# Kernel optimization log

Hardware: AMD Instinct MI355X
Metric: run time of the kernel (lower is better)

Reference implementation:

```python
import jax, jax.numpy as jnp
import numpy as np

D_MODEL = 2048
NUM_HEADS = 32
NUM_KV_HEADS = 8
D_K = D_MODEL // NUM_HEADS
B, S = 2, 2048


def setup_inputs() -> dict:
    key = jax.random.key(0)
    ks = jax.random.split(key, 6)
    sc = 1.0 / np.sqrt(D_MODEL)
    x = jax.random.normal(ks[0], (B, S, D_MODEL), dtype=jnp.float32)
    mask = jnp.tril(jnp.ones((S, S), dtype=jnp.float32))[None, None]  # [1,1,S,S]
    return {
        'x': x,
        'mask': mask,
        'Wq': jax.random.normal(ks[1], (D_MODEL, D_MODEL), jnp.float32) * sc,
        'bq': jnp.zeros((D_MODEL,), jnp.float32),
        'Wk': jax.random.normal(ks[2], (D_MODEL, NUM_KV_HEADS * D_K), jnp.float32) * sc,
        'bk': jnp.zeros((NUM_KV_HEADS * D_K,), jnp.float32),
        'Wv': jax.random.normal(ks[3], (D_MODEL, NUM_KV_HEADS * D_K), jnp.float32) * sc,
        'bv': jnp.zeros((NUM_KV_HEADS * D_K,), jnp.float32),
        'Wo': jax.random.normal(ks[4], (D_MODEL, D_MODEL), jnp.float32) * sc,
        'bo': jnp.zeros((D_MODEL,), jnp.float32),
    }


def reference(x, mask, Wq, bq, Wk, bk, Wv, bv, Wo, bo):
    b, s, _ = x.shape
    g = NUM_HEADS // NUM_KV_HEADS  # queries per kv head
    Q = (x @ Wq + bq).reshape(b, s, NUM_HEADS, D_K).transpose(0, 2, 1, 3)      # [b,h,s,dk]
    K = (x @ Wk + bk).reshape(b, s, NUM_KV_HEADS, D_K).transpose(0, 2, 1, 3)   # [b,kv,s,dk]
    V = (x @ Wv + bv).reshape(b, s, NUM_KV_HEADS, D_K).transpose(0, 2, 1, 3)
    # group queries per kv head instead of repeat_interleave on K/V
    Qg = Q.reshape(b, NUM_KV_HEADS, g, s, D_K)
    scores = jnp.einsum('bkgqd,bkld->bkgql', Qg, K) / np.sqrt(D_K)             # [b,kv,g,s,s]
    scores = jnp.where(mask[:, :, None] == 0, -1e9, scores)
    attn = jax.nn.softmax(scores, axis=-1)
    out = jnp.einsum('bkgql,bkld->bkgqd', attn, V)                              # [b,kv,g,s,dk]
    out = out.reshape(b, NUM_HEADS, s, D_K).transpose(0, 2, 1, 3).reshape(b, s, D_MODEL)
    return out @ Wo + bo
```

## Files before the change

### kernel.cpp

```cpp
#include <hip/hip_runtime.h>
#include <stdint.h>

typedef __bf16 bf16x8 __attribute__((ext_vector_type(8)));
typedef float  f32x4  __attribute__((ext_vector_type(4)));

__device__ __forceinline__ f32x4 mfma16(bf16x8 a, bf16x8 b, f32x4 c) {
    return __builtin_amdgcn_mfma_f32_16x16x32_bf16(a, b, c, 0, 0, 0);
}

__device__ __forceinline__ uint16_t f2bf(float f) {
    union { __bf16 b; uint16_t u; } cv; cv.b = (__bf16)f; return cv.u;
}

typedef __attribute__((address_space(3))) void as3_void;
typedef __attribute__((address_space(1))) void as1_void;
__device__ __forceinline__ void async_ld16(const void* g, void* l) {
    __builtin_amdgcn_global_load_lds((const as1_void*)g, (as3_void*)l, 16, 0, 0);
}


__global__ void convert_f32_bf16(const float* __restrict__ in, uint16_t* __restrict__ out, int n) {
    int i = (blockIdx.x * 256 + threadIdx.x) * 4;
    if (i >= n) return;
    float4 v = *(const float4*)(in + i);
    ushort4 o;
    o.x = f2bf(v.x); o.y = f2bf(v.y); o.z = f2bf(v.z); o.w = f2bf(v.w);
    *(ushort4*)(out + i) = o;
}

__global__ void transpose_f32_bf16(const float* __restrict__ in, uint16_t* __restrict__ out,
                                   int ldin, int out_off, int ldout) {
    __shared__ float tile[32][33];
    const int c0 = blockIdx.x << 5, r0 = blockIdx.y << 5;
    const int tx = threadIdx.x, ty = threadIdx.y;
#pragma unroll
    for (int i = 0; i < 4; ++i)
        tile[ty + i * 8][tx] = in[(size_t)(r0 + ty + i * 8) * ldin + c0 + tx];
    __syncthreads();
#pragma unroll
    for (int i = 0; i < 4; ++i)
        out[(size_t)(out_off + c0 + ty + i * 8) * ldout + r0 + tx] = f2bf(tile[tx][ty + i * 8]);
}

__global__ void transpose_v(const uint16_t* __restrict__ qkv, uint16_t* __restrict__ vt) {
    __shared__ uint16_t tile[32][33];
    const int c0 = blockIdx.x << 5, r0 = blockIdx.y << 5, b = blockIdx.z;
    const int tx = threadIdx.x, ty = threadIdx.y;
#pragma unroll
    for (int i = 0; i < 4; ++i)
        tile[ty + i * 8][tx] = qkv[(size_t)(b * 2048 + r0 + ty + i * 8) * 3072 + 2560 + c0 + tx];
    __syncthreads();
    const int perm = 4 * (tx >> 3) + (((tx & 7) < 4) ? 0 : 16) + (tx & 3);
#pragma unroll
    for (int i = 0; i < 4; ++i)
        vt[(size_t)(b * 512 + c0 + ty + i * 8) * 2048 + r0 + tx] = tile[perm][ty + i * 8];
}

__global__ void concat_bias(const float* __restrict__ bq, const float* __restrict__ bk,
                            const float* __restrict__ bv, float* __restrict__ out) {
    int i = blockIdx.x * 256 + threadIdx.x;
    if (i >= 3072) return;
    out[i] = (i < 2048) ? bq[i] : (i < 2560 ? bk[i - 2048] : bv[i - 2560]);
}

template <bool F32OUT>
__global__ __launch_bounds__(256, 2)
void gemm_bt(const uint16_t* __restrict__ A, const uint16_t* __restrict__ Bt,
             const float* __restrict__ bias, void* __restrict__ Cout, int N, int K) {
    __shared__ __align__(16) uint16_t As[4096];
    __shared__ __align__(16) uint16_t Bs[4096];
    const int tid = threadIdx.x;
    const int wv = tid >> 6, ln = tid & 63;
    const int quad = ln >> 4, l16 = ln & 15;
    const int row0 = blockIdx.y << 7, col0 = blockIdx.x << 7;
    const int wm = wv >> 1, wn = wv & 1;

    const int p0 = tid, p1 = tid + 256;
    const int ar0 = p0 >> 2, ac0 = (p0 & 3) ^ ((ar0 ^ (ar0 >> 2)) & 3);
    const int ar1 = p1 >> 2, ac1 = (p1 & 3) ^ ((ar1 ^ (ar1 >> 2)) & 3);
    const uint16_t* gA0 = A + (size_t)(row0 + ar0) * K + (ac0 << 3);
    const uint16_t* gA1 = A + (size_t)(row0 + ar1) * K + (ac1 << 3);
    const uint16_t* gB0 = Bt + (size_t)(col0 + ar0) * K + (ac0 << 3);
    const uint16_t* gB1 = Bt + (size_t)(col0 + ar1) * K + (ac1 << 3);
    uint16_t* lA0 = As + (wv << 9);
    uint16_t* lA1 = As + 2048 + (wv << 9);
    uint16_t* lB0 = Bs + (wv << 9);
    uint16_t* lB1 = Bs + 2048 + (wv << 9);

    int a_off[4], b_off[4];
#pragma unroll
    for (int t = 0; t < 4; ++t) {
        int r = (wm << 6) + (t << 4) + l16;
        a_off[t] = (((r << 2) + (quad ^ ((r ^ (r >> 2)) & 3))) << 3);
        r = (wn << 6) + (t << 4) + l16;
        b_off[t] = (((r << 2) + (quad ^ ((r ^ (r >> 2)) & 3))) << 3);
    }

    f32x4 acc[4][4] = {};

    for (int k0 = 0; k0 < K; k0 += 32) {
        __syncthreads();
        async_ld16(gA0 + k0, lA0);
        async_ld16(gA1 + k0, lA1);
        async_ld16(gB0 + k0, lB0);
        async_ld16(gB1 + k0, lB1);
        __syncthreads();
        bf16x8 af[4], bfr[4];
#pragma unroll
        for (int t = 0; t < 4; ++t) af[t] = *(const bf16x8*)(As + a_off[t]);
#pragma unroll
        for (int t = 0; t < 4; ++t) bfr[t] = *(const bf16x8*)(Bs + b_off[t]);
#pragma unroll
        for (int mt = 0; mt < 4; ++mt)
#pragma unroll
            for (int nt = 0; nt < 4; ++nt)
                acc[mt][nt] = mfma16(af[mt], bfr[nt], acc[mt][nt]);
    }

#pragma unroll
    for (int nt = 0; nt < 4; ++nt) {
        const int col = col0 + (wn << 6) + (nt << 4) + l16;
        const float bv = bias[col];
#pragma unroll
        for (int mt = 0; mt < 4; ++mt) {
            const int rbase = row0 + (wm << 6) + (mt << 4) + (quad << 2);
#pragma unroll
            for (int r = 0; r < 4; ++r) {
                float v = acc[mt][nt][r] + bv;
                if (F32OUT)
                    ((float*)Cout)[(size_t)(rbase + r) * N + col] = v;
                else
                    ((uint16_t*)Cout)[(size_t)(rbase + r) * N + col] = f2bf(v);
            }
        }
    }
}

__global__ __launch_bounds__(256, 4)
void attn_fwd(const uint16_t* __restrict__ QKV, const uint16_t* __restrict__ Vt,
              uint16_t* __restrict__ AO) {
    __shared__ __align__(16) uint16_t Ks[3][2048];
    __shared__ __align__(16) uint16_t Vs[3][2048];
    __shared__ __align__(16) uint16_t Ot[4][1088];

    const int tid = threadIdx.x;
    const int wv = tid >> 6, ln = tid & 63;
    const int quad = ln >> 4, l16 = ln & 15;
    const int p = blockIdx.x, kvh = blockIdx.y, b = blockIdx.z;
    const int h = kvh * 4 + wv;

    const uint16_t* Kg = QKV + (size_t)(b * 2048) * 3072 + 2048 + kvh * 64;
    const uint16_t* Vg = Vt + (size_t)(b * 512 + kvh * 64) * 2048;

    const int kr = tid >> 3, kc = (tid & 7) ^ (kr & 7);
    const int vr = tid >> 2, vc = (tid & 3) ^ ((vr ^ (vr >> 2)) & 3);
    const uint16_t* KgT = Kg + (size_t)kr * 3072 + kc * 8;
    const uint16_t* VgT = Vg + (size_t)vr * 2048 + vc * 8;
    const int sdst = wv << 9;

    int kf_off[2][2], vf_off[4];
#pragma unroll
    for (int nt = 0; nt < 2; ++nt)
#pragma unroll
        for (int kk = 0; kk < 2; ++kk) {
            int r = nt * 16 + l16, c = kk * 4 + quad;
            kf_off[nt][kk] = ((r << 3) + (c ^ (r & 7))) << 3;
        }
#pragma unroll
    for (int nt = 0; nt < 4; ++nt) {
        int r = nt * 16 + l16;
        vf_off[nt] = ((r << 2) + (quad ^ ((r ^ (r >> 2)) & 3))) << 3;
    }

#pragma unroll
    for (int half = 0; half < 2; ++half) {
        const int w = half ? (127 - p) : p;
        const int q0 = w << 4;
        const int nkb = (w >> 1) + 1;

        bf16x8 qf[2];
#pragma unroll
        for (int kk = 0; kk < 2; ++kk)
            qf[kk] = *(const bf16x8*)(QKV +
                (size_t)(b * 2048 + q0 + l16) * 3072 + h * 64 + kk * 32 + quad * 8);

        f32x4 acc[4] = {};
        float lp = 0.0f;

        __syncthreads();
        async_ld16(KgT, Ks[0] + sdst);
        async_ld16(VgT, Vs[0] + sdst);
        __syncthreads();
        if (nkb > 1) {
            async_ld16(KgT + (size_t)32 * 3072, Ks[1] + sdst);
            async_ld16(VgT + 32, Vs[1] + sdst);
        }

        f32x4 s0 = {0.f, 0.f, 0.f, 0.f}, s1 = {0.f, 0.f, 0.f, 0.f};
        {
            bf16x8 k00 = *(const bf16x8*)(Ks[0] + kf_off[0][0]);
            bf16x8 k01 = *(const bf16x8*)(Ks[0] + kf_off[0][1]);
            bf16x8 k10 = *(const bf16x8*)(Ks[0] + kf_off[1][0]);
            bf16x8 k11 = *(const bf16x8*)(Ks[0] + kf_off[1][1]);
            s0 = mfma16(k00, qf[0], s0); s0 = mfma16(k01, qf[1], s0);
            s1 = mfma16(k10, qf[0], s1); s1 = mfma16(k11, qf[1], s1);
        }

        int cur = 0, nxt = 1, pf2 = 2;
        for (int t = 0; t < nkb - 1; ++t) {
            __syncthreads();
            if (t + 2 < nkb) {
                async_ld16(KgT + (size_t)((t + 2) << 5) * 3072, Ks[pf2] + sdst);
                async_ld16(VgT + ((t + 2) << 5), Vs[pf2] + sdst);
            }
            bf16x8 vf[4];
#pragma unroll
            for (int nt = 0; nt < 4; ++nt)
                vf[nt] = *(const bf16x8*)(Vs[cur] + vf_off[nt]);
            bf16x8 k00 = *(const bf16x8*)(Ks[nxt] + kf_off[0][0]);
            bf16x8 k01 = *(const bf16x8*)(Ks[nxt] + kf_off[0][1]);
            bf16x8 k10 = *(const bf16x8*)(Ks[nxt] + kf_off[1][0]);
            bf16x8 k11 = *(const bf16x8*)(Ks[nxt] + kf_off[1][1]);

            float e0 = __expf(fmaf(s0[0], 0.125f, -16.0f));
            float e1 = __expf(fmaf(s0[1], 0.125f, -16.0f));
            float e2 = __expf(fmaf(s0[2], 0.125f, -16.0f));
            float e3 = __expf(fmaf(s0[3], 0.125f, -16.0f));
            float e4 = __expf(fmaf(s1[0], 0.125f, -16.0f));
            float e5 = __expf(fmaf(s1[1], 0.125f, -16.0f));
            float e6 = __expf(fmaf(s1[2], 0.125f, -16.0f));
            float e7 = __expf(fmaf(s1[3], 0.125f, -16.0f));
            lp += ((e0 + e1) + (e2 + e3)) + ((e4 + e5) + (e6 + e7));
            bf16x8 pf;
            pf[0] = (__bf16)e0; pf[1] = (__bf16)e1; pf[2] = (__bf16)e2; pf[3] = (__bf16)e3;
            pf[4] = (__bf16)e4; pf[5] = (__bf16)e5; pf[6] = (__bf16)e6; pf[7] = (__bf16)e7;

            f32x4 n0 = {0.f, 0.f, 0.f, 0.f}, n1 = {0.f, 0.f, 0.f, 0.f};
            n0 = mfma16(k00, qf[0], n0); n0 = mfma16(k01, qf[1], n0);
            n1 = mfma16(k10, qf[0], n1); n1 = mfma16(k11, qf[1], n1);

#pragma unroll
            for (int nt = 0; nt < 4; ++nt)
                acc[nt] = mfma16(vf[nt], pf, acc[nt]);

            s0 = n0; s1 = n1;
            int o = cur; cur = nxt; nxt = pf2; pf2 = o;
        }

        {
            const int key0 = (nkb - 1) << 5;
            bf16x8 vf[4];
#pragma unroll
            for (int nt = 0; nt < 4; ++nt)
                vf[nt] = *(const bf16x8*)(Vs[cur] + vf_off[nt]);
            const int qrow = q0 + l16;
            float e[8];
#pragma unroll
            for (int r = 0; r < 4; ++r) {
                float v0 = __expf(fmaf(s0[r], 0.125f, -16.0f));
                float v1 = __expf(fmaf(s1[r], 0.125f, -16.0f));
                if (key0 + quad * 4 + r > qrow) v0 = 0.0f;
                if (key0 + 16 + quad * 4 + r > qrow) v1 = 0.0f;
                e[r] = v0; e[4 + r] = v1;
            }
            lp += ((e[0] + e[1]) + (e[2] + e[3])) + ((e[4] + e[5]) + (e[6] + e[7]));
            bf16x8 pf;
#pragma unroll
            for (int j = 0; j < 8; ++j) pf[j] = (__bf16)e[j];
#pragma unroll
            for (int nt = 0; nt < 4; ++nt)
                acc[nt] = mfma16(vf[nt], pf, acc[nt]);
        }

        float rs = lp;
        rs += __shfl_xor(rs, 16, 64);
        rs += __shfl_xor(rs, 32, 64);
        const float inv = 1.0f / rs;

        uint16_t* ot = Ot[wv];
#pragma unroll
        for (int nt = 0; nt < 4; ++nt)
#pragma unroll
            for (int pp = 0; pp < 2; ++pp) {
                uint32_t pk = (uint32_t)f2bf(acc[nt][2 * pp] * inv) |
                              ((uint32_t)f2bf(acc[nt][2 * pp + 1] * inv) << 16);
                *(uint32_t*)(ot + l16 * 68 + nt * 16 + quad * 4 + 2 * pp) = pk;
            }
        const int orow = ln >> 2, oc = ln & 3;
        uint4 o1 = *(const uint4*)(ot + orow * 68 + oc * 8);
        uint4 o2 = *(const uint4*)(ot + orow * 68 + (4 + oc) * 8);
        uint16_t* aobase = AO + (size_t)(b * 2048 + q0 + orow) * 2048 + h * 64;
        *(uint4*)(aobase + oc * 8) = o1;
        *(uint4*)(aobase + (4 + oc) * 8) = o2;
    }
}


extern "C" void kernel_launch(void* const* d_in, const int* in_sizes, int n_in,
                              void* d_out, int out_size, void* d_ws, size_t ws_size,
                              hipStream_t stream) {
    (void)in_sizes; (void)n_in; (void)out_size; (void)ws_size;
    const float* x  = (const float*)d_in[0];
    const float* Wq = (const float*)d_in[2];
    const float* bq = (const float*)d_in[3];
    const float* Wk = (const float*)d_in[4];
    const float* bk = (const float*)d_in[5];
    const float* Wv = (const float*)d_in[6];
    const float* bv = (const float*)d_in[7];
    const float* Wo = (const float*)d_in[8];
    const float* bo = (const float*)d_in[9];

    char* ws = (char*)d_ws;
    uint16_t* xb    = (uint16_t*)ws;
    uint16_t* wqkvT = (uint16_t*)(ws + 16777216);
    uint16_t* woT   = (uint16_t*)(ws + 16777216 + 12582912);
    float*    biasq = (float*)(ws + 16777216 + 12582912 + 8388608);
    uint16_t* qkv   = (uint16_t*)d_out;
    uint16_t* ao    = xb;
    uint16_t* vt    = wqkvT;

    dim3 tb(32, 8);
    convert_f32_bf16<<<8192, 256, 0, stream>>>(x, xb, 4096 * 2048);
    transpose_f32_bf16<<<dim3(64, 64), tb, 0, stream>>>(Wq, wqkvT, 2048, 0,    2048);
    transpose_f32_bf16<<<dim3(16, 64), tb, 0, stream>>>(Wk, wqkvT, 512,  2048, 2048);
    transpose_f32_bf16<<<dim3(16, 64), tb, 0, stream>>>(Wv, wqkvT, 512,  2560, 2048);
    transpose_f32_bf16<<<dim3(64, 64), tb, 0, stream>>>(Wo, woT,   2048, 0,    2048);
    concat_bias<<<12, 256, 0, stream>>>(bq, bk, bv, biasq);

    gemm_bt<false><<<dim3(24, 32), 256, 0, stream>>>(xb, wqkvT, biasq, qkv, 3072, 2048);
    transpose_v<<<dim3(16, 64, 2), tb, 0, stream>>>(qkv, vt);
    attn_fwd<<<dim3(64, 8, 2), 256, 0, stream>>>(qkv, vt, ao);
    gemm_bt<true><<<dim3(16, 32), 256, 0, stream>>>(ao, woT, bo, d_out, 2048, 2048);
}
```

Baseline: 323.4 us.

## Merge prep kernels, deepen GEMM K-tile, load attention K/V directly into registers

Folds the x conversion and bias concatenation into one kernel, and the four weight transposes into one launch, cutting launch count. The GEMM K step grows from 32 to 64 with a wider XOR swizzle, halving the barriers per unit of work at the cost of doubled LDS use. The attention kernel drops LDS staging of K and V: each wave reads its fragments straight from global memory into double-buffered registers, prefetching two blocks ahead. This removes block-wide syncs, but each of the four waves now loads the same K/V separately, and the launch bound occupancy drops from 4 to 3.

```diff
diff --git a/kernel.cpp b/kernel.cpp
--- a/kernel.cpp
+++ b/kernel.cpp
@@ -19,18 +19,32 @@
 }
 
 
-__global__ void convert_f32_bf16(const float* __restrict__ in, uint16_t* __restrict__ out, int n) {
-    int i = (blockIdx.x * 256 + threadIdx.x) * 4;
-    if (i >= n) return;
-    float4 v = *(const float4*)(in + i);
-    ushort4 o;
-    o.x = f2bf(v.x); o.y = f2bf(v.y); o.z = f2bf(v.z); o.w = f2bf(v.w);
-    *(ushort4*)(out + i) = o;
-}
-
-__global__ void transpose_f32_bf16(const float* __restrict__ in, uint16_t* __restrict__ out,
-                                   int ldin, int out_off, int ldout) {
+__global__ void convert_bias(const float* __restrict__ in, uint16_t* __restrict__ out,
+                             const float* __restrict__ bq, const float* __restrict__ bk,
+                             const float* __restrict__ bv, float* __restrict__ biasq) {
+    if (blockIdx.x < 8192) {
+        int i = (blockIdx.x * 256 + threadIdx.x) * 4;
+        float4 v = *(const float4*)(in + i);
+        ushort4 o;
+        o.x = f2bf(v.x); o.y = f2bf(v.y); o.z = f2bf(v.z); o.w = f2bf(v.w);
+        *(ushort4*)(out + i) = o;
+    } else {
+        int i = (blockIdx.x - 8192) * 256 + threadIdx.x;
+        if (i < 3072)
+            biasq[i] = (i < 2048) ? bq[i] : (i < 2560 ? bk[i - 2048] : bv[i - 2560]);
+    }
+}
+
+__global__ void transpose_w(const float* __restrict__ Wq, const float* __restrict__ Wk,
+                            const float* __restrict__ Wv, const float* __restrict__ Wo,
+                            uint16_t* __restrict__ wqkvT, uint16_t* __restrict__ woT) {
     __shared__ float tile[32][33];
+    const int z = blockIdx.z;
+    const float* in; uint16_t* out; int ldin, off;
+    if (z == 0)      { in = Wq; out = wqkvT; ldin = 2048; off = 0; }
+    else if (z == 1) { if (blockIdx.x >= 16) return; in = Wk; out = wqkvT; ldin = 512; off = 2048; }
+    else if (z == 2) { if (blockIdx.x >= 16) return; in = Wv; out = wqkvT; ldin = 512; off = 2560; }
+    else             { in = Wo; out = woT;   ldin = 2048; off = 0; }
     const int c0 = blockIdx.x << 5, r0 = blockIdx.y << 5;
     const int tx = threadIdx.x, ty = threadIdx.y;
 #pragma unroll
@@ -39,7 +53,7 @@
     __syncthreads();
 #pragma unroll
     for (int i = 0; i < 4; ++i)
-        out[(size_t)(out_off + c0 + ty + i * 8) * ldout + r0 + tx] = f2bf(tile[tx][ty + i * 8]);
+        out[(size_t)(off + c0 + ty + i * 8) * 2048 + r0 + tx] = f2bf(tile[tx][ty + i * 8]);
 }
 
 __global__ void transpose_v(const uint16_t* __restrict__ qkv, uint16_t* __restrict__ vt) {
@@ -56,65 +70,62 @@
         vt[(size_t)(b * 512 + c0 + ty + i * 8) * 2048 + r0 + tx] = tile[perm][ty + i * 8];
 }
 
-__global__ void concat_bias(const float* __restrict__ bq, const float* __restrict__ bk,
-                            const float* __restrict__ bv, float* __restrict__ out) {
-    int i = blockIdx.x * 256 + threadIdx.x;
-    if (i >= 3072) return;
-    out[i] = (i < 2048) ? bq[i] : (i < 2560 ? bk[i - 2048] : bv[i - 2560]);
-}
-
 template <bool F32OUT>
 __global__ __launch_bounds__(256, 2)
 void gemm_bt(const uint16_t* __restrict__ A, const uint16_t* __restrict__ Bt,
              const float* __restrict__ bias, void* __restrict__ Cout, int N, int K) {
-    __shared__ __align__(16) uint16_t As[4096];
-    __shared__ __align__(16) uint16_t Bs[4096];
+    __shared__ __align__(16) uint16_t As[8192];
+    __shared__ __align__(16) uint16_t Bs[8192];
     const int tid = threadIdx.x;
     const int wv = tid >> 6, ln = tid & 63;
     const int quad = ln >> 4, l16 = ln & 15;
     const int row0 = blockIdx.y << 7, col0 = blockIdx.x << 7;
     const int wm = wv >> 1, wn = wv & 1;
 
-    const int p0 = tid, p1 = tid + 256;
-    const int ar0 = p0 >> 2, ac0 = (p0 & 3) ^ ((ar0 ^ (ar0 >> 2)) & 3);
-    const int ar1 = p1 >> 2, ac1 = (p1 & 3) ^ ((ar1 ^ (ar1 >> 2)) & 3);
-    const uint16_t* gA0 = A + (size_t)(row0 + ar0) * K + (ac0 << 3);
-    const uint16_t* gA1 = A + (size_t)(row0 + ar1) * K + (ac1 << 3);
-    const uint16_t* gB0 = Bt + (size_t)(col0 + ar0) * K + (ac0 << 3);
-    const uint16_t* gB1 = Bt + (size_t)(col0 + ar1) * K + (ac1 << 3);
-    uint16_t* lA0 = As + (wv << 9);
-    uint16_t* lA1 = As + 2048 + (wv << 9);
-    uint16_t* lB0 = Bs + (wv << 9);
-    uint16_t* lB1 = Bs + 2048 + (wv << 9);
-
-    int a_off[4], b_off[4];
-#pragma unroll
-    for (int t = 0; t < 4; ++t) {
-        int r = (wm << 6) + (t << 4) + l16;
-        a_off[t] = (((r << 2) + (quad ^ ((r ^ (r >> 2)) & 3))) << 3);
-        r = (wn << 6) + (t << 4) + l16;
-        b_off[t] = (((r << 2) + (quad ^ ((r ^ (r >> 2)) & 3))) << 3);
-    }
+    const uint16_t* gA[4];
+    const uint16_t* gB[4];
+#pragma unroll
+    for (int j = 0; j < 4; ++j) {
+        int p = j * 256 + tid;
+        int r = p >> 3, c = (p & 7) ^ ((r ^ (r >> 3)) & 7);
+        gA[j] = A + (size_t)(row0 + r) * K + (c << 3);
+        gB[j] = Bt + (size_t)(col0 + r) * K + (c << 3);
+    }
+
+    int a_off[4][2], b_off[4][2];
+#pragma unroll
+    for (int t = 0; t < 4; ++t)
+#pragma unroll
+        for (int s = 0; s < 2; ++s) {
+            int r = (wm << 6) + (t << 4) + l16;
+            a_off[t][s] = (((r << 3) + ((4 * s + quad) ^ ((r ^ (r >> 3)) & 7))) << 3);
+            r = (wn << 6) + (t << 4) + l16;
+            b_off[t][s] = (((r << 3) + ((4 * s + quad) ^ ((r ^ (r >> 3)) & 7))) << 3);
+        }
 
     f32x4 acc[4][4] = {};
 
-    for (int k0 = 0; k0 < K; k0 += 32) {
+    for (int k0 = 0; k0 < K; k0 += 64) {
         __syncthreads();
-        async_ld16(gA0 + k0, lA0);
-        async_ld16(gA1 + k0, lA1);
-        async_ld16(gB0 + k0, lB0);
-        async_ld16(gB1 + k0, lB1);
+#pragma unroll
+        for (int j = 0; j < 4; ++j) {
+            async_ld16(gA[j] + k0, As + (j << 11) + (wv << 9));
+            async_ld16(gB[j] + k0, Bs + (j << 11) + (wv << 9));
+        }
         __syncthreads();
-        bf16x8 af[4], bfr[4];
-#pragma unroll
-        for (int t = 0; t < 4; ++t) af[t] = *(const bf16x8*)(As + a_off[t]);
-#pragma unroll
-        for (int t = 0; t < 4; ++t) bfr[t] = *(const bf16x8*)(Bs + b_off[t]);
-#pragma unroll
-        for (int mt = 0; mt < 4; ++mt)
-#pragma unroll
-            for (int nt = 0; nt < 4; ++nt)
-                acc[mt][nt] = mfma16(af[mt], bfr[nt], acc[mt][nt]);
+#pragma unroll
+        for (int s = 0; s < 2; ++s) {
+            bf16x8 af[4], bfr[4];
+#pragma unroll
+            for (int t = 0; t < 4; ++t) af[t] = *(const bf16x8*)(As + a_off[t][s]);
+#pragma unroll
+            for (int t = 0; t < 4; ++t) bfr[t] = *(const bf16x8*)(Bs + b_off[t][s]);
+#pragma unroll
+            for (int mt = 0; mt < 4; ++mt)
+#pragma unroll
+                for (int nt = 0; nt < 4; ++nt)
+                    acc[mt][nt] = mfma16(af[mt], bfr[nt], acc[mt][nt]);
+        }
     }
 
 #pragma unroll
@@ -136,11 +147,9 @@
     }
 }
 
-__global__ __launch_bounds__(256, 4)
+__global__ __launch_bounds__(256, 3)
 void attn_fwd(const uint16_t* __restrict__ QKV, const uint16_t* __restrict__ Vt,
               uint16_t* __restrict__ AO) {
-    __shared__ __align__(16) uint16_t Ks[3][2048];
-    __shared__ __align__(16) uint16_t Vs[3][2048];
     __shared__ __align__(16) uint16_t Ot[4][1088];
 
     const int tid = threadIdx.x;
@@ -149,28 +158,8 @@
     const int p = blockIdx.x, kvh = blockIdx.y, b = blockIdx.z;
     const int h = kvh * 4 + wv;
 
-    const uint16_t* Kg = QKV + (size_t)(b * 2048) * 3072 + 2048 + kvh * 64;
-    const uint16_t* Vg = Vt + (size_t)(b * 512 + kvh * 64) * 2048;
-
-    const int kr = tid >> 3, kc = (tid & 7) ^ (kr & 7);
-    const int vr = tid >> 2, vc = (tid & 3) ^ ((vr ^ (vr >> 2)) & 3);
-    const uint16_t* KgT = Kg + (size_t)kr * 3072 + kc * 8;
-    const uint16_t* VgT = Vg + (size_t)vr * 2048 + vc * 8;
-    const int sdst = wv << 9;
-
-    int kf_off[2][2], vf_off[4];
-#pragma unroll
-    for (int nt = 0; nt < 2; ++nt)
-#pragma unroll
-        for (int kk = 0; kk < 2; ++kk) {
-            int r = nt * 16 + l16, c = kk * 4 + quad;
-            kf_off[nt][kk] = ((r << 3) + (c ^ (r & 7))) << 3;
-        }
-#pragma unroll
-    for (int nt = 0; nt < 4; ++nt) {
-        int r = nt * 16 + l16;
-        vf_off[nt] = ((r << 2) + (quad ^ ((r ^ (r >> 2)) & 3))) << 3;
-    }
+    const uint16_t* Kb = QKV + ((size_t)(b * 2048) + l16) * 3072 + 2048 + kvh * 64 + quad * 8;
+    const uint16_t* Vb = Vt + ((size_t)(b * 512) + kvh * 64 + l16) * 2048 + quad * 8;
 
 #pragma unroll
     for (int half = 0; half < 2; ++half) {
@@ -187,90 +176,77 @@
         f32x4 acc[4] = {};
         float lp = 0.0f;
 
-        __syncthreads();
-        async_ld16(KgT, Ks[0] + sdst);
-        async_ld16(VgT, Vs[0] + sdst);
-        __syncthreads();
-        if (nkb > 1) {
-            async_ld16(KgT + (size_t)32 * 3072, Ks[1] + sdst);
-            async_ld16(VgT + 32, Vs[1] + sdst);
-        }
-
-        f32x4 s0 = {0.f, 0.f, 0.f, 0.f}, s1 = {0.f, 0.f, 0.f, 0.f};
-        {
-            bf16x8 k00 = *(const bf16x8*)(Ks[0] + kf_off[0][0]);
-            bf16x8 k01 = *(const bf16x8*)(Ks[0] + kf_off[0][1]);
-            bf16x8 k10 = *(const bf16x8*)(Ks[0] + kf_off[1][0]);
-            bf16x8 k11 = *(const bf16x8*)(Ks[0] + kf_off[1][1]);
-            s0 = mfma16(k00, qf[0], s0); s0 = mfma16(k01, qf[1], s0);
-            s1 = mfma16(k10, qf[0], s1); s1 = mfma16(k11, qf[1], s1);
-        }
-
-        int cur = 0, nxt = 1, pf2 = 2;
-        for (int t = 0; t < nkb - 1; ++t) {
-            __syncthreads();
-            if (t + 2 < nkb) {
-                async_ld16(KgT + (size_t)((t + 2) << 5) * 3072, Ks[pf2] + sdst);
-                async_ld16(VgT + ((t + 2) << 5), Vs[pf2] + sdst);
-            }
-            bf16x8 vf[4];
-#pragma unroll
-            for (int nt = 0; nt < 4; ++nt)
-                vf[nt] = *(const bf16x8*)(Vs[cur] + vf_off[nt]);
-            bf16x8 k00 = *(const bf16x8*)(Ks[nxt] + kf_off[0][0]);
-            bf16x8 k01 = *(const bf16x8*)(Ks[nxt] + kf_off[0][1]);
-            bf16x8 k10 = *(const bf16x8*)(Ks[nxt] + kf_off[1][0]);
-            bf16x8 k11 = *(const bf16x8*)(Ks[nxt] + kf_off[1][1]);
-
-            float e0 = __expf(fmaf(s0[0], 0.125f, -16.0f));
-            float e1 = __expf(fmaf(s0[1], 0.125f, -16.0f));
-            float e2 = __expf(fmaf(s0[2], 0.125f, -16.0f));
-            float e3 = __expf(fmaf(s0[3], 0.125f, -16.0f));
-            float e4 = __expf(fmaf(s1[0], 0.125f, -16.0f));
-            float e5 = __expf(fmaf(s1[1], 0.125f, -16.0f));
-            float e6 = __expf(fmaf(s1[2], 0.125f, -16.0f));
-            float e7 = __expf(fmaf(s1[3], 0.125f, -16.0f));
-            lp += ((e0 + e1) + (e2 + e3)) + ((e4 + e5) + (e6 + e7));
-            bf16x8 pf;
-            pf[0] = (__bf16)e0; pf[1] = (__bf16)e1; pf[2] = (__bf16)e2; pf[3] = (__bf16)e3;
-            pf[4] = (__bf16)e4; pf[5] = (__bf16)e5; pf[6] = (__bf16)e6; pf[7] = (__bf16)e7;
-
-            f32x4 n0 = {0.f, 0.f, 0.f, 0.f}, n1 = {0.f, 0.f, 0.f, 0.f};
-            n0 = mfma16(k00, qf[0], n0); n0 = mfma16(k01, qf[1], n0);
-            n1 = mfma16(k10, qf[0], n1); n1 = mfma16(k11, qf[1], n1);
-
-#pragma unroll
-            for (int nt = 0; nt < 4; ++nt)
-                acc[nt] = mfma16(vf[nt], pf, acc[nt]);
-
-            s0 = n0; s1 = n1;
-            int o = cur; cur = nxt; nxt = pf2; pf2 = o;
-        }
-
-        {
-            const int key0 = (nkb - 1) << 5;
-            bf16x8 vf[4];
-#pragma unroll
-            for (int nt = 0; nt < 4; ++nt)
-                vf[nt] = *(const bf16x8*)(Vs[cur] + vf_off[nt]);
-            const int qrow = q0 + l16;
-            float e[8];
-#pragma unroll
-            for (int r = 0; r < 4; ++r) {
-                float v0 = __expf(fmaf(s0[r], 0.125f, -16.0f));
-                float v1 = __expf(fmaf(s1[r], 0.125f, -16.0f));
-                if (key0 + quad * 4 + r > qrow) v0 = 0.0f;
-                if (key0 + 16 + quad * 4 + r > qrow) v1 = 0.0f;
-                e[r] = v0; e[4 + r] = v1;
-            }
-            lp += ((e[0] + e[1]) + (e[2] + e[3])) + ((e[4] + e[5]) + (e[6] + e[7]));
-            bf16x8 pf;
-#pragma unroll
-            for (int j = 0; j < 8; ++j) pf[j] = (__bf16)e[j];
-#pragma unroll
-            for (int nt = 0; nt < 4; ++nt)
-                acc[nt] = mfma16(vf[nt], pf, acc[nt]);
-        }
+        bf16x8 kA[4], vA[4], kB[4], vB[4];
+#define LOAD_K(j, K4)                                                              \
+        {   const uint16_t* kp = Kb + (size_t)((j) << 5) * 3072;                   \
+            K4[0] = *(const bf16x8*)(kp);                                          \
+            K4[1] = *(const bf16x8*)(kp + 32);                                     \
+            K4[2] = *(const bf16x8*)(kp + (size_t)16 * 3072);                      \
+            K4[3] = *(const bf16x8*)(kp + (size_t)16 * 3072 + 32); }
+#define LOAD_V(j, V4)                                                              \
+        {   const uint16_t* vp = Vb + ((j) << 5);                                  \
+            V4[0] = *(const bf16x8*)(vp);                                          \
+            V4[1] = *(const bf16x8*)(vp + (size_t)16 * 2048);                      \
+            V4[2] = *(const bf16x8*)(vp + (size_t)32 * 2048);                      \
+            V4[3] = *(const bf16x8*)(vp + (size_t)48 * 2048); }
+#define BODY(t, K4, V4)                                                            \
+        {   f32x4 s0 = {0.f, 0.f, 0.f, 0.f}, s1 = {0.f, 0.f, 0.f, 0.f};           \
+            s0 = mfma16(K4[0], qf[0], s0); s0 = mfma16(K4[1], qf[1], s0);          \
+            s1 = mfma16(K4[2], qf[0], s1); s1 = mfma16(K4[3], qf[1], s1);          \
+            if ((t) + 2 < nkb) LOAD_K((t) + 2, K4);                                \
+            float e0 = __expf(fmaf(s0[0], 0.125f, -16.0f));                        \
+            float e1 = __expf(fmaf(s0[1], 0.125f, -16.0f));                        \
+            float e2 = __expf(fmaf(s0[2], 0.125f, -16.0f));                        \
+            float e3 = __expf(fmaf(s0[3], 0.125f, -16.0f));                        \
+            float e4 = __expf(fmaf(s1[0], 0.125f, -16.0f));                        \
+            float e5 = __expf(fmaf(s1[1], 0.125f, -16.0f));                        \
+            float e6 = __expf(fmaf(s1[2], 0.125f, -16.0f));                        \
+            float e7 = __expf(fmaf(s1[3], 0.125f, -16.0f));                        \
+            lp += ((e0 + e1) + (e2 + e3)) + ((e4 + e5) + (e6 + e7));               \
+            bf16x8 pf;                                                             \
+            pf[0] = (__bf16)e0; pf[1] = (__bf16)e1; pf[2] = (__bf16)e2;            \
+            pf[3] = (__bf16)e3; pf[4] = (__bf16)e4; pf[5] = (__bf16)e5;            \
+            pf[6] = (__bf16)e6; pf[7] = (__bf16)e7;                                \
+            acc[0] = mfma16(V4[0], pf, acc[0]);                                    \
+            acc[1] = mfma16(V4[1], pf, acc[1]);                                    \
+            acc[2] = mfma16(V4[2], pf, acc[2]);                                    \
+            acc[3] = mfma16(V4[3], pf, acc[3]);                                    \
+            if ((t) + 2 < nkb) LOAD_V((t) + 2, V4); }
+#define TAIL(K4, V4)                                                               \
+        {   const int key0 = (nkb - 1) << 5;                                       \
+            f32x4 s0 = {0.f, 0.f, 0.f, 0.f}, s1 = {0.f, 0.f, 0.f, 0.f};            \
+            s0 = mfma16(K4[0], qf[0], s0); s0 = mfma16(K4[1], qf[1], s0);          \
+            s1 = mfma16(K4[2], qf[0], s1); s1 = mfma16(K4[3], qf[1], s1);          \
+            const int qrow = q0 + l16;                                             \
+            float e[8];                                                            \
+            _Pragma("unroll")                                                      \
+            for (int r = 0; r < 4; ++r) {                                          \
+                float v0 = __expf(fmaf(s0[r], 0.125f, -16.0f));                    \
+                float v1 = __expf(fmaf(s1[r], 0.125f, -16.0f));                    \
+                if (key0 + quad * 4 + r > qrow) v0 = 0.0f;                         \
+                if (key0 + 16 + quad * 4 + r > qrow) v1 = 0.0f;                    \
+                e[r] = v0; e[4 + r] = v1;                                          \
+            }                                                                      \
+            lp += ((e[0] + e[1]) + (e[2] + e[3])) + ((e[4] + e[5]) + (e[6] + e[7]));\
+            bf16x8 pf;                                                             \
+            _Pragma("unroll")                                                      \
+            for (int jj = 0; jj < 8; ++jj) pf[jj] = (__bf16)e[jj];                 \
+            acc[0] = mfma16(V4[0], pf, acc[0]);                                    \
+            acc[1] = mfma16(V4[1], pf, acc[1]);                                    \
+            acc[2] = mfma16(V4[2], pf, acc[2]);                                    \
+            acc[3] = mfma16(V4[3], pf, acc[3]); }
+
+        LOAD_K(0, kA); LOAD_V(0, vA);
+        if (nkb > 1) { LOAD_K(1, kB); LOAD_V(1, vB); }
+
+        int t = 0;
+        for (; t + 1 < nkb - 1; t += 2) {
+            BODY(t, kA, vA);
+            BODY(t + 1, kB, vB);
+        }
+        if (t < nkb - 1) BODY(t, kA, vA);
+
+        if ((nkb - 1) & 1) { TAIL(kB, vB); } else { TAIL(kA, vA); }
 
         float rs = lp;
         rs += __shfl_xor(rs, 16, 64);
@@ -293,6 +269,10 @@
         *(uint4*)(aobase + oc * 8) = o1;
         *(uint4*)(aobase + (4 + oc) * 8) = o2;
     }
+#undef LOAD_K
+#undef LOAD_V
+#undef BODY
+#undef TAIL
 }
 
 
@@ -320,13 +300,8 @@
     uint16_t* vt    = wqkvT;
 
     dim3 tb(32, 8);
-    convert_f32_bf16<<<8192, 256, 0, stream>>>(x, xb, 4096 * 2048);
-    transpose_f32_bf16<<<dim3(64, 64), tb, 0, stream>>>(Wq, wqkvT, 2048, 0,    2048);
-    transpose_f32_bf16<<<dim3(16, 64), tb, 0, stream>>>(Wk, wqkvT, 512,  2048, 2048);
-    transpose_f32_bf16<<<dim3(16, 64), tb, 0, stream>>>(Wv, wqkvT, 512,  2560, 2048);
-    transpose_f32_bf16<<<dim3(64, 64), tb, 0, stream>>>(Wo, woT,   2048, 0,    2048);
-    concat_bias<<<12, 256, 0, stream>>>(bq, bk, bv, biasq);
-
+    convert_bias<<<8204, 256, 0, stream>>>(x, xb, bq, bk, bv, biasq);
+    transpose_w<<<dim3(64, 64, 4), tb, 0, stream>>>(Wq, Wk, Wv, Wo, wqkvT, woT);
     gemm_bt<false><<<dim3(24, 32), 256, 0, stream>>>(xb, wqkvT, biasq, qkv, 3072, 2048);
     transpose_v<<<dim3(16, 64, 2), tb, 0, stream>>>(qkv, vt);
     attn_fwd<<<dim3(64, 8, 2), 256, 0, stream>>>(qkv, vt, ao);
```

After: 463.1 us. +43.2%, slower.
